# Kernel tuning notes

Measured on AMD Instinct MI355X. Metric: run time of the kernel, lower is better.

## Reference

```python
import jax, jax.numpy as jnp
import numpy as np

B, C, H, W = 4, 64, 96, 384
EPS = 1e-6  # LayerNorm2d eps (NAFNet)


def _ln2d(x, w, b):
    # LayerNorm over channel dim of [B,C,H,W]
    mu = jnp.mean(x, axis=1, keepdims=True)
    var = jnp.mean((x - mu) ** 2, axis=1, keepdims=True)
    xn = (x - mu) * jax.lax.rsqrt(var + EPS)
    return xn * w[None, :, None, None] + b[None, :, None, None]


def _conv1x1(x, w, b):
    # x:[B,C,H,W], w:[O,C], b:[O]
    return jnp.einsum('bchw,oc->bohw', x, w) + b[None, :, None, None]


def _l1(a, b):
    return jnp.mean(jnp.abs(a - b))


def setup_inputs() -> dict:
    key = jax.random.key(0)
    ks = jax.random.split(key, 16)
    f32 = jnp.float32
    inp = {
        'x_l': jax.random.normal(ks[0], (B, C, H, W), f32),
        'x_r': jax.random.normal(ks[1], (B, C, H, W), f32),
        'LR_left': jax.random.uniform(ks[2], (B, 3, H, W), f32),
        'LR_right': jax.random.uniform(ks[3], (B, 3, H, W), f32),
        'loss': jnp.zeros((), f32),
        'norm_l_w': jnp.ones((C,), f32), 'norm_l_b': jnp.zeros((C,), f32),
        'norm_r_w': jnp.ones((C,), f32), 'norm_r_b': jnp.zeros((C,), f32),
        'l_proj1_w': jax.random.normal(ks[4], (C, C), f32) * 0.05,
        'l_proj1_b': jnp.zeros((C,), f32),
        'r_proj1_w': jax.random.normal(ks[5], (C, C), f32) * 0.05,
        'r_proj1_b': jnp.zeros((C,), f32),
        'l_proj2_w': jax.random.normal(ks[6], (C, C), f32) * 0.05,
        'l_proj2_b': jnp.zeros((C,), f32),
        'r_proj2_w': jax.random.normal(ks[7], (C, C), f32) * 0.05,
        'r_proj2_b': jnp.zeros((C,), f32),
        # beta/gamma are zero-init in the module; use small random values so
        # the cross-attention path contributes to the output for testing.
        'beta': jax.random.normal(ks[8], (1, C, 1, 1), f32) * 0.1,
        'gamma': jax.random.normal(ks[9], (1, C, 1, 1), f32) * 0.1,
    }
    return inp


def reference(x_l, x_r, LR_left, LR_right, loss,
              norm_l_w, norm_l_b, norm_r_w, norm_r_b,
              l_proj1_w, l_proj1_b, r_proj1_w, r_proj1_b,
              l_proj2_w, l_proj2_b, r_proj2_w, r_proj2_b,
              beta, gamma):
    b, c, h, w = x_l.shape
    scale = c ** (-0.5)

    Q_l = _conv1x1(_ln2d(x_l, norm_l_w, norm_l_b), l_proj1_w, l_proj1_b)  # [b,c,h,w]
    Q_r = _conv1x1(_ln2d(x_r, norm_r_w, norm_r_b), r_proj1_w, r_proj1_b)
    V_l = _conv1x1(x_l, l_proj2_w, l_proj2_b).transpose(0, 2, 3, 1)  # [b,h,w,c]
    V_r = _conv1x1(x_r, r_proj2_w, r_proj2_b).transpose(0, 2, 3, 1)

    # per-row cross attention: [b,h,w,w]
    attention = jnp.einsum('bchw,bchv->bhwv', Q_l, Q_r) * scale
    M_r2l = jax.nn.softmax(attention, axis=-1)
    M_l2r = jax.nn.softmax(attention.transpose(0, 1, 3, 2), axis=-1)

    # validity masks (detached). NOTE: skimage morphologic_process is a
    # CPU post-process; approximated here by the raw threshold mask.
    V_l2r = jax.lax.stop_gradient((jnp.sum(M_l2r, axis=2) > 0.1)
                                  .astype(x_l.dtype).reshape(b, 1, h, w))
    V_r2l = jax.lax.stop_gradient((jnp.sum(M_r2l, axis=2) > 0.1)
                                  .astype(x_l.dtype).reshape(b, 1, h, w))

    M_lrl = jnp.einsum('bhwv,bhvu->bhwu', M_r2l, M_l2r)
    M_rlr = jnp.einsum('bhwv,bhvu->bhwu', M_l2r, M_r2l)

    F_r2l = jnp.einsum('bhwv,bhvc->bhwc', M_r2l, V_r).transpose(0, 3, 1, 2) * beta
    F_l2r = jnp.einsum('bhwv,bhvc->bhwc', M_l2r, V_l).transpose(0, 3, 1, 2) * gamma

    loss_h = _l1(M_r2l[:, :-1], M_r2l[:, 1:]) + _l1(M_l2r[:, :-1], M_l2r[:, 1:])
    loss_w = (_l1(M_r2l[:, :, :-1, :-1], M_r2l[:, :, 1:, 1:])
              + _l1(M_l2r[:, :, :-1, :-1], M_l2r[:, :, 1:, 1:]))
    loss_smooth = loss_w + loss_h

    eye = jnp.eye(w, dtype=x_l.dtype)[None, None]  # [1,1,w,w]
    m_l2r = V_l2r.transpose(0, 2, 1, 3)  # [b,h,1,w]
    m_r2l = V_r2l.transpose(0, 2, 1, 3)
    loss_cycle = (_l1(M_lrl * m_l2r, eye * m_l2r)
                  + _l1(M_rlr * m_r2l, eye * m_r2l))

    LR_r_warp = jnp.einsum('bhwv,bhvc->bhwc', M_r2l,
                           LR_right.transpose(0, 2, 3, 1)).transpose(0, 3, 1, 2)
    LR_l_warp = jnp.einsum('bhwv,bhvc->bhwc', M_l2r,
                           LR_left.transpose(0, 2, 3, 1)).transpose(0, 3, 1, 2)
    loss_photo = (_l1(LR_left * V_l2r, LR_r_warp * V_l2r)
                  + _l1(LR_right * V_r2l, LR_l_warp * V_r2l))

    loss_out = loss + 0.0025 * (loss_photo + 0.1 * loss_smooth + loss_cycle)
    return (x_l + F_r2l, x_r + F_l2r, LR_left, LR_right, loss_out)
```

## Files before the change

kernel.cpp:

```cpp
#include <hip/hip_runtime.h>
#include <hip/hip_bf16.h>

#define BB 4
#define CC 64
#define HH 96
#define WW 384
#define HW (HH*WW)
#define CHW (CC*HW)
#define BH (BB*HH)
#define EPSV 1e-6f
#define QSCALE 0.125f

typedef __hip_bfloat16 bf16;
typedef short s8vec __attribute__((ext_vector_type(8)));
typedef float f4vec __attribute__((ext_vector_type(4)));

__device__ __forceinline__ float b2f(bf16 v){ return __bfloat162float(v); }
__device__ __forceinline__ bf16 f2b(float v){ return __float2bfloat16(v); }
__device__ __forceinline__ unsigned short f2bu(float f){
    bf16 h = __float2bfloat16(f);
    return __builtin_bit_cast(unsigned short, h);
}
__device__ __forceinline__ float bfu2f(unsigned short u){
    unsigned v = ((unsigned)u)<<16;
    return __builtin_bit_cast(float, v);
}

#define ACHUNK ((size_t)HH*WW*WW)
#define SST ((size_t)BH*WW)
#define QELEMS ((size_t)HW*64)

#define SWZ(row) ((((row) + ((row)>>3)) & 7))

__global__ void k0_zero(double* dsum){
    if (threadIdx.x < 4) dsum[threadIdx.x] = 0.0;
}

__global__ __launch_bounds__(256) void k_qv(
    const float* __restrict__ xl, const float* __restrict__ xr,
    const float* __restrict__ nlw, const float* __restrict__ nlb,
    const float* __restrict__ nrw, const float* __restrict__ nrb,
    const float* __restrict__ P1l, const float* __restrict__ b1l,
    const float* __restrict__ P1r, const float* __restrict__ b1r,
    const float* __restrict__ P2l, const float* __restrict__ b2l,
    const float* __restrict__ P2r, const float* __restrict__ b2r,
    bf16* __restrict__ Ql, bf16* __restrict__ Qr,
    bf16* __restrict__ Vl, bf16* __restrict__ Vr, int b)
{
    __shared__ float xs[64*64];
    __shared__ float p1s[64*65], p2s[64*65];
    __shared__ float nws[64], nbs[64], b1s[64], b2s[64];
    __shared__ float mus[64], ris[64];
    int t = threadIdx.x;
    int wt = blockIdx.x, l = blockIdx.y;
    int w0 = wt*64;

    for (int side=0; side<2; side++){
        const float* x  = side ? xr  : xl;
        const float* nw = side ? nrw : nlw;
        const float* nb = side ? nrb : nlb;
        const float* P1 = side ? P1r : P1l;
        const float* B1 = side ? b1r : b1l;
        const float* P2 = side ? P2r : P2l;
        const float* B2 = side ? b2r : b2l;
        bf16* Q = side ? Qr : Ql;
        bf16* V = side ? Vr : Vl;
        float qsc = side ? 1.f : QSCALE;

        if (t < 64){ nws[t]=nw[t]; nbs[t]=nb[t]; b1s[t]=B1[t]; b2s[t]=B2[t]; }
        for (int k=0;k<16;k++){
            int i=t+256*k; int o=i>>6, c=i&63;
            p1s[o*65+c]=P1[i]; p2s[o*65+c]=P2[i];
        }
        const float* xb = x + (size_t)b*CHW + (size_t)l*WW + w0;
        for (int k=0;k<16;k++){
            int c=(t>>6)+4*k, w=t&63;
            xs[c*64+w] = xb[(size_t)c*HW + w];
        }
        __syncthreads();
        if (t < 64){
            float s=0.f, ss=0.f;
            for (int c=0;c<64;c++){ float v=xs[c*64+t]; s+=v; ss+=v*v; }
            float mu=s*(1.f/64.f), var=ss*(1.f/64.f)-mu*mu;
            mus[t]=mu; ris[t]=rsqrtf(var+EPSV);
        }
        __syncthreads();

        {
            int vq=t&15, ov=t>>4;
            float acc[4][4]={};
            for (int c=0;c<64;c++){
                float xv[4];
                for (int j=0;j<4;j++) xv[j]=xs[c*64+vq*4+j];
                for (int i=0;i<4;i++){
                    float w2=p2s[(ov*4+i)*65+c];
                    for (int j=0;j<4;j++) acc[i][j]+=w2*xv[j];
                }
            }
            for (int i=0;i<4;i++){
                int c=ov*4+i;
                ushort4 pk;
                pk.x=f2bu(acc[i][0]+b2s[c]); pk.y=f2bu(acc[i][1]+b2s[c]);
                pk.z=f2bu(acc[i][2]+b2s[c]); pk.w=f2bu(acc[i][3]+b2s[c]);
                *reinterpret_cast<ushort4*>(&V[(size_t)c*HW + (size_t)l*WW + w0 + vq*4]) = pk;
            }
        }
        {
            int cq=t&15, wq=t>>4;
            float muj[4], rij[4];
            for (int j=0;j<4;j++){ muj[j]=mus[wq*4+j]; rij[j]=ris[wq*4+j]; }
            float acc[4][4]={};
            for (int c=0;c<64;c++){
                float nwc=nws[c], nbc=nbs[c];
                float xn[4];
                for (int j=0;j<4;j++) xn[j]=(xs[c*64+wq*4+j]-muj[j])*rij[j]*nwc+nbc;
                for (int i=0;i<4;i++){
                    float w1=p1s[(cq*4+i)*65+c];
                    for (int j=0;j<4;j++) acc[i][j]+=w1*xn[j];
                }
            }
            for (int j=0;j<4;j++){
                int w=w0+wq*4+j;
                ushort4 pk;
                pk.x=f2bu(qsc*(acc[0][j]+b1s[cq*4+0]));
                pk.y=f2bu(qsc*(acc[1][j]+b1s[cq*4+1]));
                pk.z=f2bu(qsc*(acc[2][j]+b1s[cq*4+2]));
                pk.w=f2bu(qsc*(acc[3][j]+b1s[cq*4+3]));
                *reinterpret_cast<ushort4*>(&Q[((size_t)l*WW + w)*64 + cq*4]) = pk;
            }
        }
        __syncthreads();
    }
}

__global__ __launch_bounds__(256) void k_attn(
    const bf16* __restrict__ Ql, const bf16* __restrict__ Qr,
    bf16* __restrict__ Abuf)
{
    __shared__ bf16 As[128*72];
    __shared__ bf16 Bs[128*72];
    int t=threadIdx.x;
    int mt=blockIdx.x, nt=blockIdx.y, l=blockIdx.z;
    const bf16* Qa = Ql + ((size_t)l*WW + mt*128)*64;
    const bf16* Qb = Qr + ((size_t)l*WW + nt*128)*64;
    for (int i=0;i<4;i++){
        int lin=t+256*i;
        int r=lin>>3, c8=lin&7;
        *reinterpret_cast<uint4*>(&As[r*72+c8*8]) =
            *reinterpret_cast<const uint4*>(&Qa[(size_t)r*64 + c8*8]);
        *reinterpret_cast<uint4*>(&Bs[r*72+c8*8]) =
            *reinterpret_cast<const uint4*>(&Qb[(size_t)r*64 + c8*8]);
    }
    __syncthreads();
    int wv=t>>6, lane=t&63;
    int m0=(wv>>1)*64, n0=(wv&1)*64;
    int ln=lane&15, cq=lane>>4;
    f4vec acc[4][4];
    #pragma unroll
    for (int m=0;m<4;m++)
        #pragma unroll
        for (int n=0;n<4;n++) acc[m][n]=(f4vec){0.f,0.f,0.f,0.f};
    #pragma unroll
    for (int kk=0;kk<2;kk++){
        s8vec a[4], bb[4];
        #pragma unroll
        for (int m=0;m<4;m++) a[m]=*reinterpret_cast<const s8vec*>(&As[(m0+m*16+ln)*72 + kk*32 + cq*8]);
        #pragma unroll
        for (int n=0;n<4;n++) bb[n]=*reinterpret_cast<const s8vec*>(&Bs[(n0+n*16+ln)*72 + kk*32 + cq*8]);
        #pragma unroll
        for (int m=0;m<4;m++)
            #pragma unroll
            for (int n=0;n<4;n++)
                acc[m][n]=__builtin_amdgcn_mfma_f32_16x16x32_bf16(a[m],bb[n],acc[m][n],0,0,0);
    }
    bf16* Ab = Abuf + (size_t)l*WW*WW;
    #pragma unroll
    for (int m=0;m<4;m++){
        #pragma unroll
        for (int r=0;r<4;r++){
            int w = mt*128 + m0 + m*16 + cq*4 + r;
            #pragma unroll
            for (int n=0;n<4;n++){
                int v = nt*128 + n0 + n*16 + ln;
                Ab[(size_t)w*WW + v] = f2b(acc[m][n][r]);
            }
        }
    }
}

__global__ __launch_bounds__(384) void k3_stats(
    const bf16* __restrict__ Abuf, float* __restrict__ rmax, float* __restrict__ irsum,
    float* __restrict__ cmax, float* __restrict__ icsum, int b)
{
    __shared__ float pm[6][64], ps[6][64];
    int t=threadIdx.x, l=blockIdx.x, seg=blockIdx.y;
    int bh=b*HH+l;
    const bf16* Ab = Abuf + (size_t)l*WW*WW;
    int lane=t&63, wid=t>>6;
    for (int w=seg*64+wid; w<seg*64+64; w+=6){
        const bf16* row=Ab+(size_t)w*WW;
        float m=-1e30f;
        for (int k=0;k<6;k++) m=fmaxf(m,b2f(row[lane+64*k]));
        for (int o=32;o;o>>=1) m=fmaxf(m,__shfl_xor(m,o,64));
        float s=0.f;
        for (int k=0;k<6;k++) s+=__expf(b2f(row[lane+64*k])-m);
        for (int o=32;o;o>>=1) s+=__shfl_xor(s,o,64);
        if (lane==0){ rmax[bh*WW+w]=m; irsum[bh*WW+w]=1.f/s; }
    }
    {
        int c=t&63, v=seg*64+c;
        float m=-1e30f;
        for (int w=wid*64; w<wid*64+64; w++) m=fmaxf(m,b2f(Ab[(size_t)w*WW+v]));
        float s=0.f;
        for (int w=wid*64; w<wid*64+64; w++) s+=__expf(b2f(Ab[(size_t)w*WW+v])-m);
        pm[wid][c]=m; ps[wid][c]=s;
    }
    __syncthreads();
    if (t<64){
        float M=-1e30f;
        for (int p=0;p<6;p++) M=fmaxf(M,pm[p][t]);
        float S=0.f;
        for (int p=0;p<6;p++) S+=ps[p][t]*__expf(pm[p][t]-M);
        cmax[bh*WW+seg*64+t]=M; icsum[bh*WW+seg*64+t]=1.f/S;
    }
}

__global__ __launch_bounds__(256) void k_mats(
    bf16* __restrict__ AP, bf16* __restrict__ LT,
    const float* __restrict__ rmax, const float* __restrict__ irsum,
    const float* __restrict__ cmax, const float* __restrict__ icsum, int b)
{
    int t=threadIdx.x, l=blockIdx.x, seg=blockIdx.y;
    int bh=b*HH+l;
    bf16* Ab  = AP + (size_t)l*WW*WW;
    bf16* LTb = LT + (size_t)l*WW*WW;
    const float* rm=rmax+(size_t)bh*WW; const float* ris=irsum+(size_t)bh*WW;
    const float* cm=cmax+(size_t)bh*WW; const float* cis=icsum+(size_t)bh*WW;
    int lane6=t&63;
    float cmv[6], civ[6];
    for (int s=0;s<6;s++){ cmv[s]=cm[s*64+lane6]; civ[s]=cis[s*64+lane6]; }
    for (int k=0;k<16;k++){
        int w = seg*64 + (t>>6) + 4*k;
        float rmw = rm[w], risw = ris[w];
        for (int s=0;s<6;s++){
            int v = s*64 + lane6;
            size_t idx = (size_t)w*WW + v;
            float a = b2f(Ab[idx]);
            Ab[idx]  = f2b(__expf(a - rmw)*risw);
            LTb[idx] = f2b(__expf(a - cmv[s])*civ[s]);
        }
    }
}

__global__ __launch_bounds__(256) void k_trans(
    const bf16* __restrict__ Pm, bf16* __restrict__ PTm)
{
    __shared__ float tile[64][65];
    int t=threadIdx.x;
    int ti=blockIdx.x, tj=blockIdx.y, l=blockIdx.z;
    const bf16* Pb = Pm + (size_t)l*WW*WW;
    bf16* PTb = PTm + (size_t)l*WW*WW;
    for (int k=0;k<16;k++){
        int r=(t>>6)+4*k, c=t&63;
        tile[r][c] = b2f(Pb[(size_t)(ti*64+r)*WW + tj*64+c]);
    }
    __syncthreads();
    for (int k=0;k<16;k++){
        int r=(t>>6)+4*k, c=t&63;
        PTb[(size_t)(tj*64+r)*WW + ti*64+c] = f2b(tile[c][r]);
    }
}

__global__ __launch_bounds__(384) void k4_masks(
    const bf16* __restrict__ Pm, const bf16* __restrict__ LTm,
    float* __restrict__ mask_r2l, float* __restrict__ mask_l2r, int b)
{
    __shared__ float pa[6][64];
    int t=threadIdx.x, l=blockIdx.x, seg=blockIdx.y;
    int bh=b*HH+l;
    const bf16* Pb  = Pm  + (size_t)l*WW*WW;
    const bf16* LTb = LTm + (size_t)l*WW*WW;
    int lane=t&63, wid=t>>6;
    {
        int c=t&63, v=seg*64+c;
        float s=0.f;
        for (int w=wid*64; w<wid*64+64; w++) s+=b2f(Pb[(size_t)w*WW+v]);
        pa[wid][c]=s;
    }
    __syncthreads();
    if (t<64){
        float S=0.f;
        for (int p=0;p<6;p++) S+=pa[p][t];
        mask_r2l[bh*WW+seg*64+t]=(S>0.1f)?1.f:0.f;
    }
    for (int u=seg*64+wid; u<seg*64+64; u+=6){
        const bf16* row=LTb+(size_t)u*WW;
        float s=0.f;
        for (int k=0;k<6;k++) s+=b2f(row[lane+64*k]);
        for (int o=32;o;o>>=1) s+=__shfl_xor(s,o,64);
        if (lane==0) mask_l2r[bh*WW+u]=(s>0.1f)?1.f:0.f;
    }
}

__global__ __launch_bounds__(256) void k5m(
    const bf16* __restrict__ Msrc, const bf16* __restrict__ VT,
    const float* __restrict__ xadd, const float* __restrict__ coef,
    float* __restrict__ outp, int b, int side)
{
    __shared__ bf16 As[64*72];
    __shared__ bf16 Bs[64*72];
    int t=threadIdx.x;
    int wt=blockIdx.x, l=blockIdx.y;
    int w0=wt*64;
    int wv=t>>6, lane=t&63;
    int cb=(wv>>1)*32, wb=(wv&1)*32;
    int ln=lane&15, cq=lane>>4;
    f4vec acc[2][2];
    #pragma unroll
    for (int m=0;m<2;m++)
        #pragma unroll
        for (int n=0;n<2;n++) acc[m][n]=(f4vec){0.f,0.f,0.f,0.f};
    const bf16* Mb = Msrc + (size_t)l*WW*WW;

    for (int vt=0;vt<6;vt++){
        int v0=vt*64;
        __syncthreads();
        for (int i=0;i<2;i++){
            int lin=t+256*i; int c=lin>>3, c8=lin&7;
            *reinterpret_cast<uint4*>(&As[c*72+c8*8]) =
                *reinterpret_cast<const uint4*>(&VT[(size_t)c*HW + (size_t)l*WW + v0 + c8*8]);
        }
        if (side==0){
            for (int i=0;i<2;i++){
                int lin=t+256*i; int r=lin>>3, c8=lin&7;
                *reinterpret_cast<uint4*>(&Bs[r*72+c8*8]) =
                    *reinterpret_cast<const uint4*>(&Mb[(size_t)(w0+r)*WW + v0 + c8*8]);
            }
        } else {
            int wl=t&63, j0=t>>6;
            for (int jj=0;jj<16;jj++){
                int j=j0+4*jj;
                Bs[wl*72+j] = Mb[(size_t)(v0+j)*WW + w0 + wl];
            }
        }
        __syncthreads();
        #pragma unroll
        for (int kk=0;kk<2;kk++){
            s8vec a[2], bb[2];
            #pragma unroll
            for (int m=0;m<2;m++) a[m]=*reinterpret_cast<const s8vec*>(&As[(cb+m*16+ln)*72+kk*32+cq*8]);
            #pragma unroll
            for (int n=0;n<2;n++) bb[n]=*reinterpret_cast<const s8vec*>(&Bs[(wb+n*16+ln)*72+kk*32+cq*8]);
            #pragma unroll
            for (int m=0;m<2;m++)
                #pragma unroll
                for (int n=0;n<2;n++)
                    acc[m][n]=__builtin_amdgcn_mfma_f32_16x16x32_bf16(a[m],bb[n],acc[m][n],0,0,0);
        }
    }
    const float* xb = xadd + (size_t)b*CHW + (size_t)l*WW + w0;
    float*      ob = outp + (size_t)b*CHW + (size_t)l*WW + w0;
    #pragma unroll
    for (int m=0;m<2;m++){
        #pragma unroll
        for (int r=0;r<4;r++){
            int c = cb + m*16 + cq*4 + r;
            float cf = coef[c];
            #pragma unroll
            for (int n=0;n<2;n++){
                int w = wb + n*16 + ln;
                ob[(size_t)c*HW + w] = xb[(size_t)c*HW + w] + cf*acc[m][n][r];
            }
        }
    }
}

__global__ __launch_bounds__(256) void k6_mfma(
    const bf16* __restrict__ Pm, const bf16* __restrict__ LTm, const bf16* __restrict__ PTm,
    const float* __restrict__ mask_r2l, const float* __restrict__ mask_l2r,
    double* __restrict__ dsum, int b)
{
    __shared__ bf16 As[2][128*64];
    __shared__ bf16 Bs[2][128*64];
    int t=threadIdx.x;
    int wg=blockIdx.x;
    int xcd = wg & 7, j = wg >> 3;
    int lgrp = j/18, tile = j - lgrp*18;
    int l = xcd + 8*lgrp;
    int which = tile/9; int xt = tile - which*9;
    int wt = xt/3, ut = xt - wt*3;
    int w0=wt*128, u0=ut*128, bh=b*HH+l;
    const float* msk = which ? (mask_r2l+(size_t)bh*WW) : (mask_l2r+(size_t)bh*WW);
    const bf16* Ap = Pm  + (size_t)l*WW*WW;
    const bf16* Lt = LTm + (size_t)l*WW*WW;
    const bf16* Bsrc = (which==0 ? LTm : PTm) + (size_t)l*WW*WW;

    int wv=t>>6, lane=t&63;
    int qr=wv>>1, qc=wv&1;
    int ln=lane&15, cq=lane>>4;

    uint4 rb[4], ra[4];
    uint4 r0[2], r1[2];

    auto stage_read = [&](int kt){
        #pragma unroll
        for (int i=0;i<4;i++){
            int lin=t+256*i; int u=lin>>3, c8=lin&7;
            rb[i] = *reinterpret_cast<const uint4*>(&Bsrc[(size_t)(u0+u)*WW + kt*64 + c8*8]);
        }
        if (which==0){
            #pragma unroll
            for (int i=0;i<4;i++){
                int lin=t+256*i; int w=lin>>3, c8=lin&7;
                ra[i] = *reinterpret_cast<const uint4*>(&Ap[(size_t)(w0+w)*WW + kt*64 + c8*8]);
            }
        } else {
            #pragma unroll
            for (int i=0;i<2;i++){
                int p=(t>>4)+16*i, wc=t&15;
                const bf16* base = &Lt[(size_t)(kt*64 + 2*p)*WW + w0 + wc*8];
                r0[i] = *reinterpret_cast<const uint4*>(base);
                r1[i] = *reinterpret_cast<const uint4*>(base + WW);
            }
        }
    };
    auto stage_write = [&](int bufi){
        bf16* bsw = Bs[bufi]; bf16* asw = As[bufi];
        #pragma unroll
        for (int i=0;i<4;i++){
            int lin=t+256*i; int u=lin>>3, c8=lin&7;
            *reinterpret_cast<uint4*>((char*)bsw + u*128 + ((c8 ^ SWZ(u))<<4)) = rb[i];
        }
        if (which==0){
            #pragma unroll
            for (int i=0;i<4;i++){
                int lin=t+256*i; int w=lin>>3, c8=lin&7;
                *reinterpret_cast<uint4*>((char*)asw + w*128 + ((c8 ^ SWZ(w))<<4)) = ra[i];
            }
        } else {
            #pragma unroll
            for (int i=0;i<2;i++){
                int p=(t>>4)+16*i, wc=t&15;
                const unsigned short* q0 = reinterpret_cast<const unsigned short*>(&r0[i]);
                const unsigned short* q1 = reinterpret_cast<const unsigned short*>(&r1[i]);
                int cb2 = p>>2, off = (p&3)*4;
                #pragma unroll
                for (int jj=0;jj<8;jj++){
                    int w = wc*8 + jj;
                    unsigned val = (unsigned)q0[jj] | ((unsigned)q1[jj]<<16);
                    *reinterpret_cast<unsigned*>((char*)asw + w*128 + ((cb2 ^ SWZ(w))<<4) + off) = val;
                }
            }
        }
    };

    f4vec acc[4][4];
    #pragma unroll
    for (int m=0;m<4;m++)
        #pragma unroll
        for (int n=0;n<4;n++) acc[m][n]=(f4vec){0.f,0.f,0.f,0.f};

    stage_read(0);
    stage_write(0);
    __syncthreads();
    int cur=0;
    for (int kt=0; kt<6; kt++){
        if (kt<5) stage_read(kt+1);
        const bf16* as = As[cur]; const bf16* bs = Bs[cur];
        #pragma unroll
        for (int kk=0;kk<2;kk++){
            s8vec a[4], bb[4];
            #pragma unroll
            for (int m=0;m<4;m++){
                int r = qr*64 + m*16 + ln;
                a[m] = *reinterpret_cast<const s8vec*>(
                    (const char*)as + r*128 + (((kk*4+cq) ^ SWZ(r))<<4));
            }
            #pragma unroll
            for (int n=0;n<4;n++){
                int u = qc*64 + n*16 + ln;
                bb[n] = *reinterpret_cast<const s8vec*>(
                    (const char*)bs + u*128 + (((kk*4+cq) ^ SWZ(u))<<4));
            }
            #pragma unroll
            for (int m=0;m<4;m++)
                #pragma unroll
                for (int n=0;n<4;n++)
                    acc[m][n]=__builtin_amdgcn_mfma_f32_16x16x32_bf16(a[m],bb[n],acc[m][n],0,0,0);
        }
        if (kt<5) stage_write(cur^1);
        __syncthreads();
        cur ^= 1;
    }

    float local = 0.f;
    #pragma unroll
    for (int n=0;n<4;n++){
        int ua = u0 + qc*64 + n*16 + ln;
        float mv = msk[ua];
        #pragma unroll
        for (int m=0;m<4;m++){
            int wbase = w0 + qr*64 + m*16 + cq*4;
            #pragma unroll
            for (int r=0;r<4;r++)
                local += mv * fabsf(acc[m][n][r] - ((ua==wbase+r)?1.f:0.f));
        }
    }
    for (int o=32;o;o>>=1) local += __shfl_xor(local,o,64);
    float* red = (float*)As;
    if (lane==0) red[wv]=local;
    __syncthreads();
    if (t==0) atomicAdd(&dsum[0], (double)(red[0]+red[1]+red[2]+red[3]));
}

__global__ __launch_bounds__(256) void k78_photo_smooth(
    const bf16* __restrict__ Pm, const bf16* __restrict__ LTm,
    const float* __restrict__ mask_r2l, const float* __restrict__ mask_l2r,
    const float* __restrict__ LRl, const float* __restrict__ LRr,
    float* __restrict__ out2, float* __restrict__ out3, double* __restrict__ dsum, int b)
{
    __shared__ unsigned short lrR[3*WW], lrL[3*WW];
    __shared__ float redP[4], redW[4], redH[4];
    int t=threadIdx.x;
    int wg=blockIdx.x;
    int xcd = wg & 7, j = wg >> 3;
    int lgrp = j/6, seg = j - lgrp*6;
    int l = xcd*12 + lgrp;
    int bh = b*HH + l;

    for (int c=0;c<3;c++){
        size_t base = ((size_t)(b*3+c)*HH + l)*WW;
        if (t < 96){
            float4 vl = *reinterpret_cast<const float4*>(&LRl[base + t*4]);
            float4 vr = *reinterpret_cast<const float4*>(&LRr[base + t*4]);
            ushort4 pl, pr;
            pl.x=f2bu(vl.x); pl.y=f2bu(vl.y); pl.z=f2bu(vl.z); pl.w=f2bu(vl.w);
            pr.x=f2bu(vr.x); pr.y=f2bu(vr.y); pr.z=f2bu(vr.z); pr.w=f2bu(vr.w);
            *reinterpret_cast<ushort4*>(&lrL[c*WW + t*4]) = pl;
            *reinterpret_cast<ushort4*>(&lrR[c*WW + t*4]) = pr;
            if (seg==0){
                *reinterpret_cast<float4*>(&out2[base + t*4]) = vl;
                *reinterpret_cast<float4*>(&out3[base + t*4]) = vr;
            }
        }
    }
    __syncthreads();

    int wid=t>>6, lane=t&63;
    int r4=lane>>4, ln=lane&15;
    const bf16* Pb  = Pm  + (size_t)l*WW*WW;
    const bf16* LTb = LTm + (size_t)l*WW*WW;
    bool dnok = (l < HH-1);
    const bf16* Pdn = Pb  + (dnok ? (size_t)WW*WW : 0);
    const bf16* Ldn = LTb + (dnok ? (size_t)WW*WW : 0);
    float fdn = dnok ? 1.f : 0.f;
    int src_same = (lane & 48) | ((ln+1)&15);
    int src_zero = (lane & 48);

    float phL=0.f, lwv=0.f, lhv=0.f;

    for (int it=0; it<4; it++){
        int w = seg*64 + wid*16 + it*4 + r4;
        int wn = (w<WW-1) ? w+1 : w;
        float fwn = (w<WW-1) ? 1.f : 0.f;
        const bf16* pr  = Pb  + (size_t)w*WW;
        const bf16* lr_ = LTb + (size_t)w*WW;
        const bf16* prn = Pb  + (size_t)wn*WW;
        const bf16* lrn = LTb + (size_t)wn*WW;
        const bf16* prd = Pdn + (size_t)w*WW;
        const bf16* lrd = Ldn + (size_t)w*WW;

        uint4 up[3], ul[3], upn[3], uln[3], upd[3], uld[3];
        #pragma unroll
        for (int i=0;i<3;i++){
            int off = 8*(ln + 16*i);
            up[i]  = *reinterpret_cast<const uint4*>(pr  + off);
            ul[i]  = *reinterpret_cast<const uint4*>(lr_ + off);
            upn[i] = *reinterpret_cast<const uint4*>(prn + off);
            uln[i] = *reinterpret_cast<const uint4*>(lrn + off);
            upd[i] = *reinterpret_cast<const uint4*>(prd + off);
            uld[i] = *reinterpret_cast<const uint4*>(lrd + off);
        }
        float pn0[3], ln0[3];
        #pragma unroll
        for (int i=0;i<3;i++){
            pn0[i] = bfu2f((unsigned short)(upn[i].x & 0xffffu));
            ln0[i] = bfu2f((unsigned short)(uln[i].x & 0xffffu));
        }

        float a0=0.f,a1=0.f,a2=0.f, d0=0.f,d1=0.f,d2=0.f;
        #pragma unroll
        for (int i=0;i<3;i++){
            const unsigned short* pu = reinterpret_cast<const unsigned short*>(&up[i]);
            const unsigned short* lu = reinterpret_cast<const unsigned short*>(&ul[i]);
            const unsigned short* pnu= reinterpret_cast<const unsigned short*>(&upn[i]);
            const unsigned short* lnu= reinterpret_cast<const unsigned short*>(&uln[i]);
            const unsigned short* pdu= reinterpret_cast<const unsigned short*>(&upd[i]);
            const unsigned short* ldu= reinterpret_cast<const unsigned short*>(&uld[i]);
            int v8 = 8*(ln+16*i);
            uint4 R0 = *reinterpret_cast<const uint4*>(&lrR[0*WW + v8]);
            uint4 R1 = *reinterpret_cast<const uint4*>(&lrR[1*WW + v8]);
            uint4 R2 = *reinterpret_cast<const uint4*>(&lrR[2*WW + v8]);
            uint4 L0 = *reinterpret_cast<const uint4*>(&lrL[0*WW + v8]);
            uint4 L1 = *reinterpret_cast<const uint4*>(&lrL[1*WW + v8]);
            uint4 L2 = *reinterpret_cast<const uint4*>(&lrL[2*WW + v8]);
            const unsigned short* r0c = reinterpret_cast<const unsigned short*>(&R0);
            const unsigned short* r1c = reinterpret_cast<const unsigned short*>(&R1);
            const unsigned short* r2c = reinterpret_cast<const unsigned short*>(&R2);
            const unsigned short* l0c = reinterpret_cast<const unsigned short*>(&L0);
            const unsigned short* l1c = reinterpret_cast<const unsigned short*>(&L1);
            const unsigned short* l2c = reinterpret_cast<const unsigned short*>(&L2);

            float pn_same = __shfl(pn0[i], src_same, 64);
            float ln_same = __shfl(ln0[i], src_same, 64);
            float pn_next = __shfl(pn0[i<2 ? i+1 : 0], src_zero, 64);
            float ln_next = __shfl(ln0[i<2 ? i+1 : 0], src_zero, 64);
            float pn_last = (ln==15) ? pn_next : pn_same;
            float ln_last = (ln==15) ? ln_next : ln_same;

            float pc[8], lc[8];
            #pragma unroll
            for (int e=0;e<8;e++){ pc[e]=bfu2f(pu[e]); lc[e]=bfu2f(lu[e]); }
            #pragma unroll
            for (int e=0;e<8;e++){
                a0 += pc[e]*bfu2f(r0c[e]); a1 += pc[e]*bfu2f(r1c[e]); a2 += pc[e]*bfu2f(r2c[e]);
                d0 += lc[e]*bfu2f(l0c[e]); d1 += lc[e]*bfu2f(l1c[e]); d2 += lc[e]*bfu2f(l2c[e]);
            }
            #pragma unroll
            for (int e=0;e<8;e++){
                lhv += fdn*(fabsf(pc[e]-bfu2f(pdu[e])) + fabsf(lc[e]-bfu2f(ldu[e])));
            }
            #pragma unroll
            for (int e=0;e<7;e++){
                lwv += fwn*(fabsf(pc[e]-bfu2f(pnu[e+1])) + fabsf(lc[e]-bfu2f(lnu[e+1])));
            }
            {
                float m = (v8+7 < WW-1) ? fwn : 0.f;
                lwv += m*(fabsf(pc[7]-pn_last) + fabsf(lc[7]-ln_last));
            }
        }
        #pragma unroll
        for (int o=8;o;o>>=1){
            a0+=__shfl_xor(a0,o,64); a1+=__shfl_xor(a1,o,64); a2+=__shfl_xor(a2,o,64);
            d0+=__shfl_xor(d0,o,64); d1+=__shfl_xor(d1,o,64); d2+=__shfl_xor(d2,o,64);
        }
        if (ln==0){
            float mkL = mask_l2r[(size_t)bh*WW+w], mkR = mask_r2l[(size_t)bh*WW+w];
            size_t lrb = ((size_t)(b*3)*HH + l)*WW + w;
            size_t chs = (size_t)HH*WW;
            float l0v=LRl[lrb], l1v=LRl[lrb+chs], l2v=LRl[lrb+2*chs];
            float r0v=LRr[lrb], r1v=LRr[lrb+chs], r2v=LRr[lrb+2*chs];
            phL += mkL*(fabsf(l0v-a0)+fabsf(l1v-a1)+fabsf(l2v-a2));
            phL += mkR*(fabsf(r0v-d0)+fabsf(r1v-d1)+fabsf(r2v-d2));
        }
    }
    for (int o=32;o;o>>=1){
        phL+=__shfl_xor(phL,o,64); lwv+=__shfl_xor(lwv,o,64); lhv+=__shfl_xor(lhv,o,64);
    }
    if (lane==0){ redP[wid]=phL; redW[wid]=lwv; redH[wid]=lhv; }
    __syncthreads();
    if (t==0){
        atomicAdd(&dsum[1], (double)(redP[0]+redP[1]+redP[2]+redP[3]));
        atomicAdd(&dsum[3], (double)(redW[0]+redW[1]+redW[2]+redW[3]));
        atomicAdd(&dsum[2], (double)(redH[0]+redH[1]+redH[2]+redH[3]));
    }
}

__global__ void k9_final(const double* __restrict__ dsum, const float* __restrict__ lossin,
                         float* __restrict__ out4)
{
    if (threadIdx.x==0){
        double cyc  = dsum[0]/(double)((size_t)BB*HH*WW*WW);
        double photo= dsum[1]/(double)((size_t)BB*3*HH*WW);
        double lhv  = dsum[2]/(double)((size_t)BB*(HH-1)*WW*WW);
        double lwv  = dsum[3]/(double)((size_t)BB*HH*(WW-1)*(WW-1));
        double res  = (double)lossin[0] + 0.0025*(photo + 0.1*(lwv+lhv) + cyc);
        out4[0]=(float)res;
    }
}

extern "C" void kernel_launch(void* const* d_in, const int* in_sizes, int n_in,
                              void* d_out, int out_size, void* d_ws, size_t ws_size,
                              hipStream_t stream)
{
    (void)in_sizes; (void)n_in; (void)out_size; (void)ws_size;
    const float* x_l  = (const float*)d_in[0];
    const float* x_r  = (const float*)d_in[1];
    const float* LRl  = (const float*)d_in[2];
    const float* LRr  = (const float*)d_in[3];
    const float* lossi= (const float*)d_in[4];
    const float* nlw  = (const float*)d_in[5];
    const float* nlb  = (const float*)d_in[6];
    const float* nrw  = (const float*)d_in[7];
    const float* nrb  = (const float*)d_in[8];
    const float* lp1w = (const float*)d_in[9];
    const float* lp1b = (const float*)d_in[10];
    const float* rp1w = (const float*)d_in[11];
    const float* rp1b = (const float*)d_in[12];
    const float* lp2w = (const float*)d_in[13];
    const float* lp2b = (const float*)d_in[14];
    const float* rp2w = (const float*)d_in[15];
    const float* rp2b = (const float*)d_in[16];
    const float* beta = (const float*)d_in[17];
    const float* gamma= (const float*)d_in[18];

    bf16* Abuf = (bf16*)d_ws;
    bf16* LTb  = Abuf + ACHUNK;
    bf16* PTb  = Abuf + 2*ACHUNK;
    float* wsf = (float*)((char*)d_ws + 3*ACHUNK*2);
    float* rmax=wsf, *irsum=wsf+SST, *cmax=wsf+2*SST, *icsum=wsf+3*SST;
    float* mask_r2l=wsf+4*SST, *mask_l2r=wsf+5*SST;
    double* dsum=(double*)(wsf+6*SST);
    bf16* Qlb = PTb;
    bf16* Qrb = PTb + QELEMS;
    bf16* Vlb = PTb + 2*QELEMS;
    bf16* Vrb = PTb + 3*QELEMS;

    float* out  = (float*)d_out;
    float* out0 = out;
    float* out1 = out + (size_t)BB*CHW;
    float* out2 = out + 2*(size_t)BB*CHW;
    float* out3 = out2 + (size_t)BB*3*HW;
    float* out4 = out3 + (size_t)BB*3*HW;

    k0_zero<<<1,64,0,stream>>>(dsum);
    for (int b=0;b<BB;b++){
        k_qv<<<dim3(6,HH),256,0,stream>>>(x_l,x_r,nlw,nlb,nrw,nrb,
                                          lp1w,lp1b,rp1w,rp1b,lp2w,lp2b,rp2w,rp2b,
                                          Qlb,Qrb,Vlb,Vrb,b);
        k_attn<<<dim3(3,3,HH),256,0,stream>>>(Qlb,Qrb,Abuf);
        k3_stats<<<dim3(HH,6),384,0,stream>>>(Abuf,rmax,irsum,cmax,icsum,b);
        k_mats<<<dim3(HH,6),256,0,stream>>>(Abuf,LTb,rmax,irsum,cmax,icsum,b);
        k4_masks<<<dim3(HH,6),384,0,stream>>>(Abuf,LTb,mask_r2l,mask_l2r,b);
        k5m<<<dim3(6,HH),256,0,stream>>>(Abuf,Vrb,x_l,beta, out0,b,0);
        k5m<<<dim3(6,HH),256,0,stream>>>(LTb, Vlb,x_r,gamma,out1,b,1);
        k_trans<<<dim3(6,6,HH),256,0,stream>>>(Abuf,PTb);
        k6_mfma<<<1728,256,0,stream>>>(Abuf,LTb,PTb,mask_r2l,mask_l2r,dsum,b);
        k78_photo_smooth<<<576,256,0,stream>>>(Abuf,LTb,mask_r2l,mask_l2r,LRl,LRr,out2,out3,dsum,b);
    }
    k9_final<<<1,64,0,stream>>>(dsum,lossi,out4);
}
```

Baseline: 1.272 ms.

## Restructure softmax stats into row-pass online column reduction and fuse mask sums

After: 1.144 ms. 1.11x faster.

```diff
diff --git a/kernel.cpp b/kernel.cpp
--- a/kernel.cpp
+++ b/kernel.cpp
@@ -188,68 +188,139 @@
     }
 }
 
-__global__ __launch_bounds__(384) void k3_stats(
+__global__ __launch_bounds__(256) void k3a(
     const bf16* __restrict__ Abuf, float* __restrict__ rmax, float* __restrict__ irsum,
-    float* __restrict__ cmax, float* __restrict__ icsum, int b)
-{
-    __shared__ float pm[6][64], ps[6][64];
+    float* __restrict__ pcm, float* __restrict__ pcs, int b)
+{
+    __shared__ float cpm[4][384], cps[4][384];
     int t=threadIdx.x, l=blockIdx.x, seg=blockIdx.y;
     int bh=b*HH+l;
     const bf16* Ab = Abuf + (size_t)l*WW*WW;
-    int lane=t&63, wid=t>>6;
-    for (int w=seg*64+wid; w<seg*64+64; w+=6){
-        const bf16* row=Ab+(size_t)w*WW;
-        float m=-1e30f;
-        for (int k=0;k<6;k++) m=fmaxf(m,b2f(row[lane+64*k]));
-        for (int o=32;o;o>>=1) m=fmaxf(m,__shfl_xor(m,o,64));
-        float s=0.f;
-        for (int k=0;k<6;k++) s+=__expf(b2f(row[lane+64*k])-m);
-        for (int o=32;o;o>>=1) s+=__shfl_xor(s,o,64);
-        if (lane==0){ rmax[bh*WW+w]=m; irsum[bh*WW+w]=1.f/s; }
-    }
-    {
-        int c=t&63, v=seg*64+c;
-        float m=-1e30f;
-        for (int w=wid*64; w<wid*64+64; w++) m=fmaxf(m,b2f(Ab[(size_t)w*WW+v]));
-        float s=0.f;
-        for (int w=wid*64; w<wid*64+64; w++) s+=__expf(b2f(Ab[(size_t)w*WW+v])-m);
-        pm[wid][c]=m; ps[wid][c]=s;
+    int wid=t>>6, lane=t&63, r4=lane>>4, ln=lane&15;
+    float cm[24], cs[24];
+    #pragma unroll
+    for (int c=0;c<24;c++){ cm[c]=-1e30f; cs[c]=0.f; }
+
+    for (int it=0; it<4; it++){
+        int w = seg*64 + wid*16 + it*4 + r4;
+        const bf16* row = Ab + (size_t)w*WW;
+        float x[24];
+        #pragma unroll
+        for (int i=0;i<3;i++){
+            uint4 u = *reinterpret_cast<const uint4*>(row + 8*(ln+16*i));
+            const unsigned short* p = reinterpret_cast<const unsigned short*>(&u);
+            #pragma unroll
+            for (int e=0;e<8;e++) x[i*8+e] = bfu2f(p[e]);
+        }
+        float m = x[0];
+        #pragma unroll
+        for (int c=1;c<24;c++) m = fmaxf(m, x[c]);
+        #pragma unroll
+        for (int o=1;o<16;o<<=1) m = fmaxf(m, __shfl_xor(m, o, 64));
+        float s = 0.f;
+        #pragma unroll
+        for (int c=0;c<24;c++) s += __expf(x[c]-m);
+        #pragma unroll
+        for (int o=1;o<16;o<<=1) s += __shfl_xor(s, o, 64);
+        if (ln==0){ rmax[(size_t)bh*WW+w]=m; irsum[(size_t)bh*WW+w]=1.f/s; }
+        #pragma unroll
+        for (int c=0;c<24;c++){
+            float mn = fmaxf(cm[c], x[c]);
+            cs[c] = cs[c]*__expf(cm[c]-mn) + __expf(x[c]-mn);
+            cm[c] = mn;
+        }
+    }
+    #pragma unroll
+    for (int o=16;o<64;o<<=1){
+        #pragma unroll
+        for (int c=0;c<24;c++){
+            float om = __shfl_xor(cm[c], o, 64);
+            float os = __shfl_xor(cs[c], o, 64);
+            float mn = fmaxf(cm[c], om);
+            cs[c] = cs[c]*__expf(cm[c]-mn) + os*__expf(om-mn);
+            cm[c] = mn;
+        }
+    }
+    if (r4==0){
+        #pragma unroll
+        for (int i=0;i<3;i++)
+            #pragma unroll
+            for (int e=0;e<8;e++){
+                cpm[wid][8*(ln+16*i)+e]=cm[i*8+e];
+                cps[wid][8*(ln+16*i)+e]=cs[i*8+e];
+            }
     }
     __syncthreads();
-    if (t<64){
-        float M=-1e30f;
-        for (int p=0;p<6;p++) M=fmaxf(M,pm[p][t]);
-        float S=0.f;
-        for (int p=0;p<6;p++) S+=ps[p][t]*__expf(pm[p][t]-M);
-        cmax[bh*WW+seg*64+t]=M; icsum[bh*WW+seg*64+t]=1.f/S;
-    }
+    for (int c=t;c<384;c+=256){
+        float M=cpm[0][c], S=cps[0][c];
+        #pragma unroll
+        for (int p2=1;p2<4;p2++){
+            float om=cpm[p2][c], os=cps[p2][c];
+            float mn=fmaxf(M,om);
+            S = S*__expf(M-mn) + os*__expf(om-mn);
+            M = mn;
+        }
+        pcm[((size_t)l*6+seg)*384+c]=M;
+        pcs[((size_t)l*6+seg)*384+c]=S;
+    }
+}
+
+__global__ __launch_bounds__(384) void k3b(
+    const float* __restrict__ pcm, const float* __restrict__ pcs,
+    float* __restrict__ cmax, float* __restrict__ icsum,
+    float* __restrict__ mr2l_acc, int b)
+{
+    int l=blockIdx.x, c=threadIdx.x, bh=b*HH+l;
+    float M=-1e30f, S=0.f;
+    for (int s=0;s<6;s++){
+        float om=pcm[((size_t)l*6+s)*384+c], os=pcs[((size_t)l*6+s)*384+c];
+        float mn=fmaxf(M,om);
+        S = S*__expf(M-mn) + os*__expf(om-mn);
+        M = mn;
+    }
+    cmax[(size_t)bh*WW+c]=M; icsum[(size_t)bh*WW+c]=1.f/S;
+    mr2l_acc[(size_t)bh*WW+c]=0.f;
 }
 
 __global__ __launch_bounds__(256) void k_mats(
     bf16* __restrict__ AP, bf16* __restrict__ LT,
     const float* __restrict__ rmax, const float* __restrict__ irsum,
-    const float* __restrict__ cmax, const float* __restrict__ icsum, int b)
-{
+    const float* __restrict__ cmax, const float* __restrict__ icsum,
+    float* __restrict__ mr2l_acc, float* __restrict__ ml2r_sum, int b)
+{
+    __shared__ float cssum[4][384];
     int t=threadIdx.x, l=blockIdx.x, seg=blockIdx.y;
     int bh=b*HH+l;
     bf16* Ab  = AP + (size_t)l*WW*WW;
     bf16* LTb = LT + (size_t)l*WW*WW;
     const float* rm=rmax+(size_t)bh*WW; const float* ris=irsum+(size_t)bh*WW;
     const float* cm=cmax+(size_t)bh*WW; const float* cis=icsum+(size_t)bh*WW;
-    int lane6=t&63;
-    float cmv[6], civ[6];
-    for (int s=0;s<6;s++){ cmv[s]=cm[s*64+lane6]; civ[s]=cis[s*64+lane6]; }
+    int wid=t>>6, lane6=t&63;
+    float cmv[6], civ[6], colp[6];
+    for (int s=0;s<6;s++){ cmv[s]=cm[s*64+lane6]; civ[s]=cis[s*64+lane6]; colp[s]=0.f; }
     for (int k=0;k<16;k++){
-        int w = seg*64 + (t>>6) + 4*k;
+        int w = seg*64 + wid + 4*k;
         float rmw = rm[w], risw = ris[w];
+        float rowp = 0.f;
         for (int s=0;s<6;s++){
             int v = s*64 + lane6;
             size_t idx = (size_t)w*WW + v;
             float a = b2f(Ab[idx]);
-            Ab[idx]  = f2b(__expf(a - rmw)*risw);
-            LTb[idx] = f2b(__expf(a - cmv[s])*civ[s]);
-        }
-    }
+            bf16 pb = f2b(__expf(a - rmw)*risw);
+            bf16 lb = f2b(__expf(a - cmv[s])*civ[s]);
+            Ab[idx]  = pb;
+            LTb[idx] = lb;
+            colp[s] += b2f(pb);
+            rowp    += b2f(lb);
+        }
+        for (int o=32;o;o>>=1) rowp += __shfl_xor(rowp,o,64);
+        if (lane6==0) ml2r_sum[(size_t)bh*WW+w] = rowp;
+    }
+    for (int s=0;s<6;s++) cssum[wid][s*64+lane6] = colp[s];
+    __syncthreads();
+    for (int c=t;c<384;c+=256)
+        atomicAdd(&mr2l_acc[(size_t)bh*WW+c],
+                  cssum[0][c]+cssum[1][c]+cssum[2][c]+cssum[3][c]);
 }
 
 __global__ __launch_bounds__(256) void k_trans(
@@ -260,45 +331,27 @@
     int ti=blockIdx.x, tj=blockIdx.y, l=blockIdx.z;
     const bf16* Pb = Pm + (size_t)l*WW*WW;
     bf16* PTb = PTm + (size_t)l*WW*WW;
-    for (int k=0;k<16;k++){
-        int r=(t>>6)+4*k, c=t&63;
-        tile[r][c] = b2f(Pb[(size_t)(ti*64+r)*WW + tj*64+c]);
+    #pragma unroll
+    for (int i=0;i<2;i++){
+        int lin=t+256*i; int r=lin>>3, c8=lin&7;
+        uint4 u = *reinterpret_cast<const uint4*>(&Pb[(size_t)(ti*64+r)*WW + tj*64 + c8*8]);
+        const unsigned short* p = reinterpret_cast<const unsigned short*>(&u);
+        #pragma unroll
+        for (int e=0;e<8;e++) tile[r][c8*8+e] = bfu2f(p[e]);
     }
     __syncthreads();
-    for (int k=0;k<16;k++){
-        int r=(t>>6)+4*k, c=t&63;
-        PTb[(size_t)(tj*64+r)*WW + ti*64+c] = f2b(tile[c][r]);
-    }
-}
-
-__global__ __launch_bounds__(384) void k4_masks(
-    const bf16* __restrict__ Pm, const bf16* __restrict__ LTm,
-    float* __restrict__ mask_r2l, float* __restrict__ mask_l2r, int b)
-{
-    __shared__ float pa[6][64];
-    int t=threadIdx.x, l=blockIdx.x, seg=blockIdx.y;
-    int bh=b*HH+l;
-    const bf16* Pb  = Pm  + (size_t)l*WW*WW;
-    const bf16* LTb = LTm + (size_t)l*WW*WW;
-    int lane=t&63, wid=t>>6;
-    {
-        int c=t&63, v=seg*64+c;
-        float s=0.f;
-        for (int w=wid*64; w<wid*64+64; w++) s+=b2f(Pb[(size_t)w*WW+v]);
-        pa[wid][c]=s;
-    }
-    __syncthreads();
-    if (t<64){
-        float S=0.f;
-        for (int p=0;p<6;p++) S+=pa[p][t];
-        mask_r2l[bh*WW+seg*64+t]=(S>0.1f)?1.f:0.f;
-    }
-    for (int u=seg*64+wid; u<seg*64+64; u+=6){
-        const bf16* row=LTb+(size_t)u*WW;
-        float s=0.f;
-        for (int k=0;k<6;k++) s+=b2f(row[lane+64*k]);
-        for (int o=32;o;o>>=1) s+=__shfl_xor(s,o,64);
-        if (lane==0) mask_l2r[bh*WW+u]=(s>0.1f)?1.f:0.f;
+    #pragma unroll
+    for (int i=0;i<2;i++){
+        int lin=t+256*i; int vr=lin>>3, c8=lin&7;
+        unsigned short o[8];
+        #pragma unroll
+        for (int e=0;e<8;e++) o[e] = f2bu(tile[c8*8+e][vr]);
+        uint4 pk;
+        pk.x = (unsigned)o[0] | ((unsigned)o[1]<<16);
+        pk.y = (unsigned)o[2] | ((unsigned)o[3]<<16);
+        pk.z = (unsigned)o[4] | ((unsigned)o[5]<<16);
+        pk.w = (unsigned)o[6] | ((unsigned)o[7]<<16);
+        *reinterpret_cast<uint4*>(&PTb[(size_t)(tj*64+vr)*WW + ti*64 + c8*8]) = pk;
     }
 }
 
@@ -497,7 +550,7 @@
     #pragma unroll
     for (int n=0;n<4;n++){
         int ua = u0 + qc*64 + n*16 + ln;
-        float mv = msk[ua];
+        float mv = (msk[ua] > 0.1f) ? 1.f : 0.f;
         #pragma unroll
         for (int m=0;m<4;m++){
             int wbase = w0 + qr*64 + m*16 + cq*4;
@@ -645,7 +698,8 @@
             d0+=__shfl_xor(d0,o,64); d1+=__shfl_xor(d1,o,64); d2+=__shfl_xor(d2,o,64);
         }
         if (ln==0){
-            float mkL = mask_l2r[(size_t)bh*WW+w], mkR = mask_r2l[(size_t)bh*WW+w];
+            float mkL = (mask_l2r[(size_t)bh*WW+w] > 0.1f) ? 1.f : 0.f;
+            float mkR = (mask_r2l[(size_t)bh*WW+w] > 0.1f) ? 1.f : 0.f;
             size_t lrb = ((size_t)(b*3)*HH + l)*WW + w;
             size_t chs = (size_t)HH*WW;
             float l0v=LRl[lrb], l1v=LRl[lrb+chs], l2v=LRl[lrb+2*chs];
@@ -715,6 +769,8 @@
     bf16* Qrb = PTb + QELEMS;
     bf16* Vlb = PTb + 2*QELEMS;
     bf16* Vrb = PTb + 3*QELEMS;
+    float* pcm = (float*)PTb;
+    float* pcs = pcm + (size_t)HH*6*384;
 
     float* out  = (float*)d_out;
     float* out0 = out;
@@ -729,9 +785,10 @@
                                           lp1w,lp1b,rp1w,rp1b,lp2w,lp2b,rp2w,rp2b,
                                           Qlb,Qrb,Vlb,Vrb,b);
         k_attn<<<dim3(3,3,HH),256,0,stream>>>(Qlb,Qrb,Abuf);
-        k3_stats<<<dim3(HH,6),384,0,stream>>>(Abuf,rmax,irsum,cmax,icsum,b);
-        k_mats<<<dim3(HH,6),256,0,stream>>>(Abuf,LTb,rmax,irsum,cmax,icsum,b);
-        k4_masks<<<dim3(HH,6),384,0,stream>>>(Abuf,LTb,mask_r2l,mask_l2r,b);
+        k3a<<<dim3(HH,6),256,0,stream>>>(Abuf,rmax,irsum,pcm,pcs,b);
+        k3b<<<HH,384,0,stream>>>(pcm,pcs,cmax,icsum,mask_r2l,b);
+        k_mats<<<dim3(HH,6),256,0,stream>>>(Abuf,LTb,rmax,irsum,cmax,icsum,
+                                            mask_r2l,mask_l2r,b);
         k5m<<<dim3(6,HH),256,0,stream>>>(Abuf,Vrb,x_l,beta, out0,b,0);
         k5m<<<dim3(6,HH),256,0,stream>>>(LTb, Vlb,x_r,gamma,out1,b,1);
         k_trans<<<dim3(6,6,HH),256,0,stream>>>(Abuf,PTb);
```
